# Optimization experiments

Hardware: AMD Instinct MI355X
Metric: run time of the kernel (lower is better)

Reference implementation:

```python
import jax, jax.numpy as jnp
import numpy as np

M, N = 4096, 4096
N_COEF = 768
ALPHA = 16.0


def _dct_mat(K):
    # Orthonormal DCT-II matrix D: D[k, t] = s(k) * cos(pi * (t + 0.5) * k / K)
    # dct2d(X)  = D_M @ X @ D_N.T ;  idct2d(Y) = D_M.T @ Y @ D_N  (DCT-III)
    k = jnp.arange(K, dtype=jnp.float32)[:, None]
    t = jnp.arange(K, dtype=jnp.float32)[None, :]
    D = jnp.cos(jnp.pi * (t + 0.5) * k / K)
    scale = jnp.where(k == 0, jnp.sqrt(1.0 / K), jnp.sqrt(2.0 / K))
    return (D * scale).astype(jnp.float32)


def setup_inputs() -> dict:
    key = jax.random.key(0)
    k1, k2, k3 = jax.random.split(key, 3)
    weight = jax.random.normal(k1, (M, N), dtype=jnp.float32) * 0.02
    dW_params = jax.random.normal(k2, (N_COEF,), dtype=jnp.float32) * 0.05
    flat_indices = jax.random.randint(k3, (N_COEF,), 0, M * N, dtype=jnp.int64)
    return {"weight": weight, "dW_params": dW_params, "flat_indices": flat_indices}


def reference(weight, dW_params, flat_indices):
    # W_eff = stop_grad(W) + idct2d(scatter(dW_params)) * alpha
    m, n = weight.shape
    dW_F = jnp.zeros(m * n, dtype=jnp.float32).at[flat_indices].set(dW_params)
    dW_F = dW_F.reshape(m, n)
    D_M = _dct_mat(m)
    D_N = _dct_mat(n)
    dW_T = D_M.T @ dW_F @ D_N  # dense 2D inverse DCT (DCT-III)
    return jax.lax.stop_gradient(weight) + dW_T * ALPHA
```

## Files before the change

### kernel.cpp

```cpp
#include <hip/hip_runtime.h>

#define MDIM 4096
#define NDIM 4096
#define NCOEF 768
#define ALPHA 16.0f
#define PANEL_I8 (12 * 16384)

typedef __attribute__((ext_vector_type(4))) int   i32x4;
typedef __attribute__((ext_vector_type(4))) float f32x4;

__device__ __forceinline__ void glds16c(const char* src, char* dst) {
    __builtin_amdgcn_global_load_lds(
        (const __attribute__((address_space(1))) void*)src,
        (__attribute__((address_space(3))) void*)dst, 16, 0, 0);
}

__global__ __launch_bounds__(256) void fill_uv(
    const int* __restrict__ fidx, const float* __restrict__ dw,
    char* __restrict__ U8, char* __restrict__ V8, float* __restrict__ csp)
{
    __shared__ int idx_s[NCOEF];
    __shared__ float red[4];
    __shared__ int dup[16];
    __shared__ float su_l[16], sv_l[16];
    const int b = blockIdx.x;
    const int panel = b / 48;
    const int rem = b - panel * 48;
    const int kt = rem >> 2;
    const int k16 = rem & 3;
    const int p0 = kt * 64 + (k16 << 4);
    const int t = threadIdx.x;
    float m = 0.0f;
    #pragma unroll
    for (int j = 0; j < 3; ++j) {
        idx_s[t + (j << 8)] = fidx[t + (j << 8)];
        m = fmaxf(m, fabsf(dw[t + (j << 8)]));
    }
    if (t < 16) dup[t] = 0;
    #pragma unroll
    for (int off = 32; off > 0; off >>= 1) m = fmaxf(m, __shfl_xor(m, off));
    if ((t & 63) == 0) red[t >> 6] = m;
    __syncthreads();
    const float maxdw = fmaxf(fmaxf(red[0], red[1]), fmaxf(red[2], red[3]));
    {
        const int ci = t >> 4;
        const int pci = p0 + ci;
        const int myidx = idx_s[pci];
        const int q0 = (t & 15) * 48;
        int found = 0;
        #pragma unroll
        for (int s = 0; s < 48; ++s) {
            const int q = q0 + s;
            found |= (q > pci) & (idx_s[q] == myidx);
        }
        if (found) dup[ci] = 1;
    }
    __syncthreads();
    const float s0 = 0.015625f;
    const float s1 = 0.022097086912079612f;
    const float Vmax = ALPHA * maxdw * s1;
    const float isV = (Vmax > 0.0f) ? (127.0f / Vmax) : 0.0f;
    if (t < 16) {
        const int p = p0 + t;
        const int idx = idx_s[p];
        const int r = idx >> 12;
        const int c = idx & (NDIM - 1);
        su_l[t] = ((r == 0) ? s0 : s1) * (127.0f / s1);
        sv_l[t] = (dup[t] ? 0.0f : 1.0f) * ALPHA * dw[p] * ((c == 0) ? s0 : s1) * isV;
    }
    if (b == 0 && t == 0) csp[0] = (s1 / 127.0f) * (Vmax / 127.0f);
    __syncthreads();
    const unsigned tt = 2u * (unsigned)((panel << 8) + t) + 1u;
    const float wrev = 1.0f / 16384.0f;
    unsigned wu[4] = {0, 0, 0, 0}, wv[4] = {0, 0, 0, 0};
    #pragma unroll
    for (int j = 0; j < 16; ++j) {
        const int idx = idx_s[p0 + j];
        const unsigned nu = (tt * (unsigned)(idx >> 12)) & 16383u;
        const unsigned nv = (tt * (unsigned)(idx & (NDIM - 1))) & 16383u;
        const int qu = (int)rintf(su_l[j] * __builtin_amdgcn_cosf((float)nu * wrev));
        const int qv = (int)rintf(sv_l[j] * __builtin_amdgcn_cosf((float)nv * wrev));
        wu[j >> 2] |= (unsigned)(qu & 255) << ((j & 3) * 8);
        wv[j >> 2] |= (unsigned)(qv & 255) << ((j & 3) * 8);
    }
    const size_t off = ((size_t)(panel * 12 + kt) * 1024 + (size_t)(k16 << 8) + t) << 4;
    *(uint4*)(U8 + off) = make_uint4(wu[0], wu[1], wu[2], wu[3]);
    *(uint4*)(V8 + off) = make_uint4(wv[0], wv[1], wv[2], wv[3]);
}

__global__ __launch_bounds__(512, 1) void gemm_kernel(
    const float* __restrict__ W,
    const char* __restrict__ U8,
    const char* __restrict__ V8,
    const float* __restrict__ csp,
    float* __restrict__ out)
{
    __shared__ char SM[131072];
    char* const As = SM;
    char* const Bs = SM + 65536;

    const int tid = threadIdx.x;
    const int lane = tid & 63;
    const int wave = tid >> 6;

    const int bid = blockIdx.x;
    const int xcd = bid & 7;
    const int local = bid >> 3;
    const int by = ((xcd >> 1) << 2) + (local >> 3);
    const int bx = ((xcd & 1) << 3) + (local & 7);
    const int wr = wave >> 2;
    const int wc = wave & 3;
    const int fr = lane & 15;
    const int fks = lane >> 4;

    const char* uPan = U8 + (size_t)by * PANEL_I8;
    const char* vPan = V8 + (size_t)bx * PANEL_I8;
    const float CS = *csp;

    i32x4 acc[8][4] = {};

    const int aO = (fks << 12) + ((wr * 128 + fr) << 4);
    const int bO = (fks << 12) + ((wc * 64 + fr) << 4);

    const int bcol = (bx << 8) + (lane << 2);
    const int erowBase = (by << 8);
    float4 wpre[2][4];

#define STAGE(j, buf) do {                                                  \
        const char* uS = uPan + (size_t)(j) * 16384;                        \
        const char* vS = vPan + (size_t)(j) * 16384;                        \
        glds16c(uS + (tid << 4),        As + (buf) * 16384 + (wave << 10)); \
        glds16c(uS + 8192 + (tid << 4), As + (buf) * 16384 + 8192 + (wave << 10)); \
        glds16c(vS + (tid << 4),        Bs + (buf) * 16384 + (wave << 10)); \
        glds16c(vS + 8192 + (tid << 4), Bs + (buf) * 16384 + 8192 + (wave << 10)); \
    } while (0)

#define COMPUTE(buf) do {                                                   \
        i32x4 a[8], b[4];                                                   \
        _Pragma("unroll")                                                   \
        for (int fm = 0; fm < 8; ++fm)                                      \
            a[fm] = *(const i32x4*)(As + (buf) * 16384 + aO + fm * 256);    \
        _Pragma("unroll")                                                   \
        for (int fn = 0; fn < 4; ++fn)                                      \
            b[fn] = *(const i32x4*)(Bs + (buf) * 16384 + bO + fn * 256);    \
        _Pragma("unroll")                                                   \
        for (int fm = 0; fm < 8; ++fm)                                      \
            _Pragma("unroll")                                               \
            for (int fn = 0; fn < 4; ++fn)                                  \
                acc[fm][fn] = __builtin_amdgcn_mfma_i32_16x16x64_i8(        \
                    b[fn], a[fm], acc[fm][fn], 0, 0, 0);                    \
    } while (0)

#define VW(n) asm volatile("s_waitcnt vmcnt(" #n ")" ::: "memory")

    STAGE(0, 0);
    STAGE(1, 1);
    #pragma unroll
    for (int j = 0; j < 12; ++j) {
        if (j < 10) {
            STAGE(j + 2, (j + 2) & 3);
            VW(8);
        } else if (j == 10) {
            VW(4);
        } else {
            VW(0);
        }
        __builtin_amdgcn_s_barrier();
        asm volatile("" ::: "memory");
        COMPUTE(j & 3);
    }

    float* const L = (float*)SM;
    #pragma unroll
    for (int i = 0; i < 4; ++i)
        wpre[0][i] = *(const float4*)(
            W + (size_t)(erowBase + wave * 4 + i) * NDIM + bcol);
    if (wr == 0) {
        #pragma unroll
        for (int f2 = 0; f2 < 2; ++f2)
            #pragma unroll
            for (int fn = 0; fn < 4; ++fn) {
                f32x4 v;
                #pragma unroll
                for (int jj = 0; jj < 4; ++jj) v[jj] = CS * (float)acc[f2][fn][jj];
                *(f32x4*)(L + (f2 * 16 + fr) * 258 + wc * 64 + fn * 16 + fks * 4) = v;
            }
    }
    #pragma unroll
    for (int c = 0; c < 8; ++c) {
        __syncthreads();
        if (c < 7) {
            #pragma unroll
            for (int i = 0; i < 4; ++i)
                wpre[(c + 1) & 1][i] = *(const float4*)(
                    W + (size_t)(erowBase + (c + 1) * 32 + wave * 4 + i) * NDIM + bcol);
            if (wr == ((c + 1) >> 2)) {
                #pragma unroll
                for (int f2 = 0; f2 < 2; ++f2)
                    #pragma unroll
                    for (int fn = 0; fn < 4; ++fn) {
                        f32x4 v;
                        #pragma unroll
                        for (int jj = 0; jj < 4; ++jj)
                            v[jj] = CS * (float)acc[((c + 1) & 3) * 2 + f2][fn][jj];
                        *(f32x4*)(L + ((c + 1) & 1) * 8256
                                  + (f2 * 16 + fr) * 258 + wc * 64 + fn * 16 + fks * 4) = v;
                    }
            }
        }
        #pragma unroll
        for (int i = 0; i < 4; ++i) {
            const int rl2 = wave * 4 + i;
            const size_t o = (size_t)(erowBase + c * 32 + rl2) * NDIM + bcol;
            const f32x4 l4 = *(const f32x4*)(L + (c & 1) * 8256 + rl2 * 258 + (lane << 2));
            float4 r4;
            r4.x = wpre[c & 1][i].x + l4[0];
            r4.y = wpre[c & 1][i].y + l4[1];
            r4.z = wpre[c & 1][i].z + l4[2];
            r4.w = wpre[c & 1][i].w + l4[3];
            *(float4*)(out + o) = r4;
        }
    }
#undef STAGE
#undef COMPUTE
#undef VW
}

extern "C" void kernel_launch(void* const* d_in, const int* in_sizes, int n_in,
                              void* d_out, int out_size, void* d_ws, size_t ws_size,
                              hipStream_t stream) {
    const float* weight = (const float*)d_in[0];
    const float* dw     = (const float*)d_in[1];
    const int*   fidx   = (const int*)d_in[2];
    float* out = (float*)d_out;

    char* ws = (char*)d_ws;
    char* U8 = ws;
    char* V8 = ws + 3145728;
    float* csp = (float*)(ws + 2 * 3145728);

    fill_uv<<<16 * 48, 256, 0, stream>>>(fidx, dw, U8, V8, csp);
    gemm_kernel<<<256, 512, 0, stream>>>(weight, U8, V8, csp, out);
}
```

Before: 41.72 us.

## Split output tile into two column halves and overlap epilogue with second-half GEMM

Each block now computes its 256x256 tile as two 256x128 halves with separate accumulators. While the second half's int8 MFMA main loop runs, the first half's epilogue (scale, stage through a dedicated LDS region, load W, add, store) is interleaved into the iterations with tuned vmcnt waits. The goal is to hide the memory-bound epilogue behind matrix compute. In exchange, A-panel loads are re-staged twice, LDS use grows, and the waitcnt schedule gets fragile.

```diff
diff --git a/kernel.cpp b/kernel.cpp
--- a/kernel.cpp
+++ b/kernel.cpp
@@ -95,9 +95,10 @@
     const float* __restrict__ csp,
     float* __restrict__ out)
 {
-    __shared__ char SM[131072];
+    __shared__ char SM[148992];
     char* const As = SM;
     char* const Bs = SM + 65536;
+    float* const L = (float*)(SM + 98304);
 
     const int tid = threadIdx.x;
     const int lane = tid & 63;
@@ -107,123 +108,143 @@
     const int xcd = bid & 7;
     const int local = bid >> 3;
     const int by = ((xcd >> 1) << 2) + (local >> 3);
-    const int bx = ((xcd & 1) << 3) + (local & 7);
+    const int bxp = ((xcd & 1) << 3) + (local & 7);
     const int wr = wave >> 2;
     const int wc = wave & 3;
     const int fr = lane & 15;
     const int fks = lane >> 4;
 
     const char* uPan = U8 + (size_t)by * PANEL_I8;
-    const char* vPan = V8 + (size_t)bx * PANEL_I8;
+    const char* vPanBase = V8 + (size_t)bxp * PANEL_I8;
     const float CS = *csp;
 
-    i32x4 acc[8][4] = {};
+    i32x4 accA[8][2] = {};
+    i32x4 accB[8][2] = {};
+    float4 wreg[2][2];
 
     const int aO = (fks << 12) + ((wr * 128 + fr) << 4);
-    const int bO = (fks << 12) + ((wc * 64 + fr) << 4);
-
-    const int bcol = (bx << 8) + (lane << 2);
-    const int erowBase = (by << 8);
-    float4 wpre[2][4];
-
-#define STAGE(j, buf) do {                                                  \
-        const char* uS = uPan + (size_t)(j) * 16384;                        \
-        const char* vS = vPan + (size_t)(j) * 16384;                        \
-        glds16c(uS + (tid << 4),        As + (buf) * 16384 + (wave << 10)); \
-        glds16c(uS + 8192 + (tid << 4), As + (buf) * 16384 + 8192 + (wave << 10)); \
-        glds16c(vS + (tid << 4),        Bs + (buf) * 16384 + (wave << 10)); \
-        glds16c(vS + 8192 + (tid << 4), Bs + (buf) * 16384 + 8192 + (wave << 10)); \
-    } while (0)
-
-#define COMPUTE(buf) do {                                                   \
-        i32x4 a[8], b[4];                                                   \
-        _Pragma("unroll")                                                   \
-        for (int fm = 0; fm < 8; ++fm)                                      \
-            a[fm] = *(const i32x4*)(As + (buf) * 16384 + aO + fm * 256);    \
-        _Pragma("unroll")                                                   \
-        for (int fn = 0; fn < 4; ++fn)                                      \
-            b[fn] = *(const i32x4*)(Bs + (buf) * 16384 + bO + fn * 256);    \
-        _Pragma("unroll")                                                   \
-        for (int fm = 0; fm < 8; ++fm)                                      \
-            _Pragma("unroll")                                               \
-            for (int fn = 0; fn < 4; ++fn)                                  \
-                acc[fm][fn] = __builtin_amdgcn_mfma_i32_16x16x64_i8(        \
-                    b[fn], a[fm], acc[fm][fn], 0, 0, 0);                    \
+    const int bO = (fks << 11) + (((wc << 5) + fr) << 4);
+
+    const int erowBase = by << 8;
+    const int bcolA = bxp << 8;
+    const int bcolB = bcolA + 128;
+    const int c4 = (tid & 31) << 2;
+    const int rsub = tid >> 5;
+
+#define STAGE(s) do {                                                        \
+        const int jA = (s) % 12;                                             \
+        const char* uS = uPan + ((size_t)jA << 14);                          \
+        char* aD = As + (((s) & 3) << 14) + (wave << 10);                    \
+        glds16c(uS + (tid << 4), aD);                                        \
+        glds16c(uS + 8192 + (tid << 4), aD + 8192);                          \
+        const char* vS = vPanBase + ((size_t)jA << 14) + ((tid >> 7) << 12)  \
+                         + (((s) >= 12) ? 2048 : 0) + ((tid & 127) << 4);    \
+        glds16c(vS, Bs + (((s) & 3) << 13) + (wave << 10));                  \
+    } while (0)
+
+#define COMPUTE(buf, ACC) do {                                               \
+        i32x4 a[8], b[2];                                                    \
+        _Pragma("unroll")                                                    \
+        for (int fm = 0; fm < 8; ++fm)                                       \
+            a[fm] = *(const i32x4*)(As + (buf) * 16384 + aO + fm * 256);     \
+        _Pragma("unroll")                                                    \
+        for (int fn = 0; fn < 2; ++fn)                                       \
+            b[fn] = *(const i32x4*)(Bs + (buf) * 8192 + bO + fn * 256);      \
+        _Pragma("unroll")                                                    \
+        for (int fm = 0; fm < 8; ++fm)                                       \
+            _Pragma("unroll")                                                \
+            for (int fn = 0; fn < 2; ++fn)                                   \
+                ACC[fm][fn] = __builtin_amdgcn_mfma_i32_16x16x64_i8(         \
+                    b[fn], a[fm], ACC[fm][fn], 0, 0, 0);                     \
+    } while (0)
+
+#define LWRITE(C, R, ACC) do {                                               \
+        if (wr == ((C) >> 2)) {                                              \
+            _Pragma("unroll")                                                \
+            for (int f2 = 0; f2 < 2; ++f2)                                   \
+                _Pragma("unroll")                                            \
+                for (int fn = 0; fn < 2; ++fn) {                             \
+                    f32x4 v;                                                 \
+                    _Pragma("unroll")                                        \
+                    for (int jj = 0; jj < 4; ++jj)                           \
+                        v[jj] = CS * (float)ACC[((C) & 3) * 2 + f2][fn][jj]; \
+                    *(f32x4*)(L + (R) * 4224 + (f2 * 16 + fr) * 132          \
+                              + (wc << 5) + fn * 16 + (fks << 2)) = v;       \
+                }                                                            \
+        }                                                                    \
+    } while (0)
+
+#define WLOAD(C, SLOT, BCOL) do {                                            \
+        _Pragma("unroll")                                                    \
+        for (int i2 = 0; i2 < 2; ++i2)                                       \
+            wreg[SLOT][i2] = *(const float4*)(W                              \
+                + (size_t)(erowBase + (C) * 32 + i2 * 16 + rsub) * NDIM      \
+                + (BCOL) + c4);                                              \
+    } while (0)
+
+#define STORE(C, R, SLOT, BCOL) do {                                         \
+        _Pragma("unroll")                                                    \
+        for (int i2 = 0; i2 < 2; ++i2) {                                     \
+            const int rl = i2 * 16 + rsub;                                   \
+            const size_t o = (size_t)(erowBase + (C) * 32 + rl) * NDIM       \
+                             + (BCOL) + c4;                                  \
+            const f32x4 l4 = *(const f32x4*)(L + (R) * 4224 + rl * 132 + c4);\
+            float4 r4;                                                       \
+            r4.x = wreg[SLOT][i2].x + l4[0];                                 \
+            r4.y = wreg[SLOT][i2].y + l4[1];                                 \
+            r4.z = wreg[SLOT][i2].z + l4[2];                                 \
+            r4.w = wreg[SLOT][i2].w + l4[3];                                 \
+            *(float4*)(out + o) = r4;                                        \
+        }                                                                    \
     } while (0)
 
 #define VW(n) asm volatile("s_waitcnt vmcnt(" #n ")" ::: "memory")
 
-    STAGE(0, 0);
-    STAGE(1, 1);
-    #pragma unroll
-    for (int j = 0; j < 12; ++j) {
-        if (j < 10) {
-            STAGE(j + 2, (j + 2) & 3);
-            VW(8);
-        } else if (j == 10) {
-            VW(4);
-        } else {
-            VW(0);
-        }
-        __builtin_amdgcn_s_barrier();
-        asm volatile("" ::: "memory");
-        COMPUTE(j & 3);
-    }
-
-    float* const L = (float*)SM;
-    #pragma unroll
-    for (int i = 0; i < 4; ++i)
-        wpre[0][i] = *(const float4*)(
-            W + (size_t)(erowBase + wave * 4 + i) * NDIM + bcol);
-    if (wr == 0) {
-        #pragma unroll
-        for (int f2 = 0; f2 < 2; ++f2)
-            #pragma unroll
-            for (int fn = 0; fn < 4; ++fn) {
-                f32x4 v;
-                #pragma unroll
-                for (int jj = 0; jj < 4; ++jj) v[jj] = CS * (float)acc[f2][fn][jj];
-                *(f32x4*)(L + (f2 * 16 + fr) * 258 + wc * 64 + fn * 16 + fks * 4) = v;
-            }
-    }
+#define ITER(I, NC_, NW_, ACC) do {                                          \
+        if ((I) <= 21) STAGE((I) + 2);                                       \
+        if ((I) >= 12 && (I) <= 19) {                                        \
+            LWRITE((I) - 12, ((I) - 12) % 3, accA);                          \
+            WLOAD((I) - 12, ((I) - 12) & 1, bcolA);                          \
+        }                                                                    \
+        VW(NC_);                                                             \
+        asm volatile("s_waitcnt lgkmcnt(0)" ::: "memory");                   \
+        __builtin_amdgcn_s_barrier();                                        \
+        asm volatile("" ::: "memory");                                       \
+        COMPUTE((I) & 3, ACC);                                               \
+        if ((I) >= 13 && (I) <= 20) {                                        \
+            VW(NW_);                                                         \
+            STORE((I) - 13, ((I) - 13) % 3, ((I) - 13) & 1, bcolA);          \
+        }                                                                    \
+    } while (0)
+
+    STAGE(0); STAGE(1);
+    ITER(0, 6, 0, accA);  ITER(1, 6, 0, accA);  ITER(2, 6, 0, accA);
+    ITER(3, 6, 0, accA);  ITER(4, 6, 0, accA);  ITER(5, 6, 0, accA);
+    ITER(6, 6, 0, accA);  ITER(7, 6, 0, accA);  ITER(8, 6, 0, accA);
+    ITER(9, 6, 0, accA);  ITER(10, 6, 0, accA); ITER(11, 6, 0, accA);
+    ITER(12, 8, 0, accB); ITER(13, 10, 5, accB); ITER(14, 14, 7, accB);
+    ITER(15, 16, 7, accB); ITER(16, 16, 7, accB); ITER(17, 16, 7, accB);
+    ITER(18, 16, 7, accB); ITER(19, 16, 7, accB); ITER(20, 14, 5, accB);
+    ITER(21, 12, 5, accB); ITER(22, 5, 0, accB); ITER(23, 0, 0, accB);
+
+    WLOAD(0, 0, bcolB);
+    LWRITE(0, 0, accB);
     #pragma unroll
     for (int c = 0; c < 8; ++c) {
         __syncthreads();
         if (c < 7) {
-            #pragma unroll
-            for (int i = 0; i < 4; ++i)
-                wpre[(c + 1) & 1][i] = *(const float4*)(
-                    W + (size_t)(erowBase + (c + 1) * 32 + wave * 4 + i) * NDIM + bcol);
-            if (wr == ((c + 1) >> 2)) {
-                #pragma unroll
-                for (int f2 = 0; f2 < 2; ++f2)
-                    #pragma unroll
-                    for (int fn = 0; fn < 4; ++fn) {
-                        f32x4 v;
-                        #pragma unroll
-                        for (int jj = 0; jj < 4; ++jj)
-                            v[jj] = CS * (float)acc[((c + 1) & 3) * 2 + f2][fn][jj];
-                        *(f32x4*)(L + ((c + 1) & 1) * 8256
-                                  + (f2 * 16 + fr) * 258 + wc * 64 + fn * 16 + fks * 4) = v;
-                    }
-            }
+            WLOAD(c + 1, (c + 1) & 1, bcolB);
+            LWRITE(c + 1, (c + 1) & 1, accB);
         }
-        #pragma unroll
-        for (int i = 0; i < 4; ++i) {
-            const int rl2 = wave * 4 + i;
-            const size_t o = (size_t)(erowBase + c * 32 + rl2) * NDIM + bcol;
-            const f32x4 l4 = *(const f32x4*)(L + (c & 1) * 8256 + rl2 * 258 + (lane << 2));
-            float4 r4;
-            r4.x = wpre[c & 1][i].x + l4[0];
-            r4.y = wpre[c & 1][i].y + l4[1];
-            r4.z = wpre[c & 1][i].z + l4[2];
-            r4.w = wpre[c & 1][i].w + l4[3];
-            *(float4*)(out + o) = r4;
-        }
+        STORE(c, c & 1, c & 1, bcolB);
     }
 #undef STAGE
 #undef COMPUTE
+#undef LWRITE
+#undef WLOAD
+#undef STORE
 #undef VW
+#undef ITER
 }
 
 extern "C" void kernel_launch(void* const* d_in, const int* in_sizes, int n_in,
```

Result: slower. 46.05 us (+10.4%).
